# Performance work log

Hardware: AMD Instinct MI355X
Metric: run time of the kernel (lower is better)

The kernel has to match this reference:

```python
import itertools
import jax, jax.numpy as jnp
import numpy as np

B, RES, H, KD, DIM = 16, (32, 32), 16, 128, 2048
N = RES[0] * RES[1]          # 1024 tokens
D = KD                       # per-head dim (attn_ratio=1)
DH = H * D                   # 2048
QKV_OUT = 3 * DH             # 6144
SCALE = KD ** -0.5
LN_EPS = 1e-5


def _make_bias_idxs():
    points = list(itertools.product(range(RES[0]), range(RES[1])))
    offsets = {}
    idxs = []
    for p1 in points:
        for p2 in points:
            off = (abs(p1[0] - p2[0]), abs(p1[1] - p2[1]))
            if off not in offsets:
                offsets[off] = len(offsets)
            idxs.append(offsets[off])
    return np.array(idxs, dtype=np.int32).reshape(N, N), len(offsets)


def setup_inputs() -> dict:
    key = jax.random.key(0)
    ks = jax.random.split(key, 6)
    idxs_np, n_off = _make_bias_idxs()  # n_off == 1024 for 32x32
    return {
        "x": jax.random.normal(ks[0], (B, N, DIM), jnp.float32),
        "ln_gamma": jnp.ones((DIM,), jnp.float32),
        "ln_beta": jnp.zeros((DIM,), jnp.float32),
        "qkv_w": jax.random.normal(ks[1], (DIM, QKV_OUT), jnp.float32) * (DIM ** -0.5),
        "qkv_b": jnp.zeros((QKV_OUT,), jnp.float32),
        "proj_w": jax.random.normal(ks[2], (DH, DIM), jnp.float32) * (DH ** -0.5),
        "proj_b": jnp.zeros((DIM,), jnp.float32),
        "attention_biases": jax.random.normal(ks[3], (H, n_off), jnp.float32) * 0.02,
        "bias_idxs": jnp.asarray(idxs_np),
    }


def reference(x, ln_gamma, ln_beta, qkv_w, qkv_b, proj_w, proj_b,
              attention_biases, bias_idxs):
    # LayerNorm over last dim
    mu = jnp.mean(x, axis=-1, keepdims=True)
    var = jnp.mean(jnp.square(x - mu), axis=-1, keepdims=True)
    xn = (x - mu) * jax.lax.rsqrt(var + LN_EPS) * ln_gamma + ln_beta

    qkv = xn @ qkv_w + qkv_b                      # [B, N, 3*H*D]
    qkv = qkv.reshape(B, N, 3, H, D).transpose(2, 0, 3, 1, 4)  # [3, B, H, N, D]
    q, k, v = qkv[0], qkv[1], qkv[2]

    attn = jnp.einsum('bhid,bhjd->bhij', q, k) * SCALE  # [B, H, N, N]
    bias = attention_biases[:, bias_idxs]               # gather -> [H, N, N]
    attn = jax.nn.softmax(attn + bias, axis=-1)

    out = jnp.einsum('bhij,bhjd->bhid', attn, v)        # [B, H, N, D]
    out = out.transpose(0, 2, 1, 3).reshape(B, N, DH)   # b n (h d)
    return out @ proj_w + proj_b
```

## Files before the change

### kernel.cpp

```cpp
#include <hip/hip_runtime.h>


typedef __attribute__((ext_vector_type(4)))  float          f32x4;
typedef __attribute__((ext_vector_type(16))) float          f32x16;
typedef __attribute__((ext_vector_type(8)))  short          bf16x8;
typedef __attribute__((ext_vector_type(8)))  unsigned short u16x8;
typedef __attribute__((ext_vector_type(4)))  unsigned short u16x4;

#define DEV __device__ __forceinline__

DEV unsigned short f2bf(float f) {
  union { float f; unsigned int u; } v; v.f = f;
  unsigned int r = v.u + 0x7fffu + ((v.u >> 16) & 1u);
  return (unsigned short)(r >> 16);
}

DEV f32x4 mfma16(bf16x8 a, bf16x8 b, f32x4 c) {
  return __builtin_amdgcn_mfma_f32_16x16x32_bf16(a, b, c, 0, 0, 0);
}
DEV f32x16 mfma32(bf16x8 a, bf16x8 b, f32x16 c) {
  return __builtin_amdgcn_mfma_f32_32x32x16_bf16(a, b, c, 0, 0, 0);
}

#define GLD_LDS16(g, l) __builtin_amdgcn_global_load_lds(                      \
    (const __attribute__((address_space(1))) void*)(g),                        \
    (__attribute__((address_space(3))) void*)(l), 16, 0, 0)

__global__ __launch_bounds__(256) void ln_kernel(
    const float* __restrict__ x, const float* __restrict__ gam,
    const float* __restrict__ bet, unsigned short* __restrict__ xn)
{
  const int row = blockIdx.x;
  const int t   = threadIdx.x;
  const f32x4* xr = (const f32x4*)(x + (size_t)row * 2048);
  f32x4 v0 = xr[t * 2], v1 = xr[t * 2 + 1];
  float s = 0.f, ss = 0.f;
#pragma unroll
  for (int i = 0; i < 4; ++i) { s += v0[i]; ss += v0[i] * v0[i]; }
#pragma unroll
  for (int i = 0; i < 4; ++i) { s += v1[i]; ss += v1[i] * v1[i]; }
#pragma unroll
  for (int off = 32; off; off >>= 1) {
    s  += __shfl_xor(s, off);
    ss += __shfl_xor(ss, off);
  }
  __shared__ float r0[4], r1[4];
  const int w = t >> 6, lane = t & 63;
  if (lane == 0) { r0[w] = s; r1[w] = ss; }
  __syncthreads();
  s  = r0[0] + r0[1] + r0[2] + r0[3];
  ss = r1[0] + r1[1] + r1[2] + r1[3];
  const float mu = s * (1.f / 2048.f);
  const float rs = rsqrtf(ss * (1.f / 2048.f) - mu * mu + 1e-5f);
  const f32x4* gr = (const f32x4*)gam;
  const f32x4* br = (const f32x4*)bet;
  f32x4 g0 = gr[t * 2], g1 = gr[t * 2 + 1];
  f32x4 b0 = br[t * 2], b1 = br[t * 2 + 1];
  u16x8 o;
#pragma unroll
  for (int i = 0; i < 4; ++i) o[i]     = f2bf((v0[i] - mu) * rs * g0[i] + b0[i]);
#pragma unroll
  for (int i = 0; i < 4; ++i) o[4 + i] = f2bf((v1[i] - mu) * rs * g1[i] + b1[i]);
  *(u16x8*)(xn + (size_t)row * 2048 + t * 8) = o;
}

__global__ __launch_bounds__(256) void wtrans(
    const float* __restrict__ W, unsigned short* __restrict__ Wt, int K, int C)
{
  __shared__ float tile[32][33];
  const int c0 = blockIdx.x * 32, k0 = blockIdx.y * 32;
  const int t = threadIdx.x;
  const int r8 = t >> 5, c32 = t & 31;
#pragma unroll
  for (int i = 0; i < 4; ++i)
    tile[i * 8 + r8][c32] = W[(size_t)(k0 + i * 8 + r8) * C + c0 + c32];
  __syncthreads();
#pragma unroll
  for (int i = 0; i < 4; ++i)
    Wt[(size_t)(c0 + i * 8 + r8) * K + k0 + c32] = f2bf(tile[c32][i * 8 + r8]);
}

template <int EPI>
__global__ __launch_bounds__(256, 2) void gemm_nt(
    const unsigned short* __restrict__ A, const unsigned short* __restrict__ Wt,
    const float* __restrict__ bias, void* __restrict__ o0,
    void* __restrict__ o1, void* __restrict__ o2, int K, int C)
{
  __shared__ unsigned short lds[2][2][8192];
  const int nwg   = gridDim.x * gridDim.y;
  const int chunk = nwg >> 3;
  int flat = blockIdx.y * gridDim.x + blockIdx.x;
  flat = (flat & 7) * chunk + (flat >> 3);
  const int m0 = (flat / gridDim.x) * 128;
  const int n0 = (flat % gridDim.x) * 128;
  const int tid = threadIdx.x, lane = tid & 63, w = tid >> 6;
  const int lhi = lane >> 4, llo = lane & 15;
  const int wr = w >> 1, wc = w & 1;

  const unsigned short* Ab = A  + (size_t)m0 * K;
  const unsigned short* Bb = Wt + (size_t)n0 * K;

  f32x4 acc[4][4];
#pragma unroll
  for (int i = 0; i < 4; ++i)
#pragma unroll
    for (int j = 0; j < 4; ++j) { acc[i][j][0] = 0; acc[i][j][1] = 0; acc[i][j][2] = 0; acc[i][j][3] = 0; }

  auto stage = [&](int kt, int buf) {
    const int k0 = kt * 64;
#pragma unroll
    for (int i = 0; i < 4; ++i) {
      const int c    = w * 4 + i;
      const int row  = c * 8 + (lane >> 3);
      const int colb = (lane & 7) * 16;
      const int scol = (colb ^ ((row & 7) << 4)) >> 1;
      GLD_LDS16(Ab + (size_t)row * K + k0 + scol, &lds[buf][0][c * 512]);
      GLD_LDS16(Bb + (size_t)row * K + k0 + scol, &lds[buf][1][c * 512]);
    }
  };

  stage(0, 0);
  __syncthreads();
  const int nk = K >> 6;
  int cur = 0;
  for (int kt = 0; kt < nk; ++kt) {
    if (kt + 1 < nk) stage(kt + 1, cur ^ 1);
    const char* aL = (const char*)&lds[cur][0][0];
    const char* bL = (const char*)&lds[cur][1][0];
#pragma unroll
    for (int kk = 0; kk < 2; ++kk) {
      const int kb = kk * 64 + lhi * 16;
      bf16x8 af[4], bf[4];
#pragma unroll
      for (int t2 = 0; t2 < 4; ++t2) {
        const int ra = wr * 64 + t2 * 16 + llo;
        af[t2] = *(const bf16x8*)(aL + ra * 128 + (kb ^ ((ra & 7) << 4)));
        const int rb = wc * 64 + t2 * 16 + llo;
        bf[t2] = *(const bf16x8*)(bL + rb * 128 + (kb ^ ((rb & 7) << 4)));
      }
#pragma unroll
      for (int ai = 0; ai < 4; ++ai)
#pragma unroll
        for (int bj = 0; bj < 4; ++bj)
          acc[ai][bj] = mfma16(af[ai], bf[bj], acc[ai][bj]);
    }
    __syncthreads();
    cur ^= 1;
  }

  if (EPI == 0) {
    unsigned short* q  = (unsigned short*)o0;
    unsigned short* kk = (unsigned short*)o1;
    unsigned short* vT = (unsigned short*)o2;
    const int which = n0 >> 11;
    const int h     = (n0 >> 7) & 15;
#pragma unroll
    for (int bj = 0; bj < 4; ++bj) {
      const int c  = n0 + wc * 64 + bj * 16 + llo;
      const float bv = bias[c];
      const int d  = c & 127;
#pragma unroll
      for (int ai = 0; ai < 4; ++ai) {
        const int m = m0 + wr * 64 + ai * 16 + lhi * 4;
        const int b = m >> 10, n = m & 1023;
        if (which == 2) {
          u16x4 pk;
#pragma unroll
          for (int r = 0; r < 4; ++r) pk[r] = f2bf(acc[ai][bj][r] + bv);
          *(u16x4*)(vT + ((size_t)(b * 16 + h) * 128 + d) * 1024 + n) = pk;
        } else {
          unsigned short* dst = (which == 0) ? q : kk;
          const float sc = (which == 0) ? 0.08838834764831845f : 1.0f;
#pragma unroll
          for (int r = 0; r < 4; ++r)
            dst[((size_t)(b * 16 + h) * 1024 + n + r) * 128 + d] =
                f2bf((acc[ai][bj][r] + bv) * sc);
        }
      }
    }
  } else {
    float* fo = (float*)o0;
#pragma unroll
    for (int bj = 0; bj < 4; ++bj) {
      const int c  = n0 + wc * 64 + bj * 16 + llo;
      const float bv = bias[c];
#pragma unroll
      for (int ai = 0; ai < 4; ++ai) {
        const int m = m0 + wr * 64 + ai * 16 + lhi * 4;
#pragma unroll
        for (int r = 0; r < 4; ++r)
          fo[(size_t)(m + r) * C + c] = acc[ai][bj][r] + bv;
      }
    }
  }
}

__global__ __launch_bounds__(256) void attn4(
    const unsigned short* __restrict__ q, const unsigned short* __restrict__ k,
    const unsigned short* __restrict__ vT, const float* __restrict__ biases,
    unsigned short* __restrict__ aout, int n_off)
{
  __shared__ unsigned short kt[2][8192];
  __shared__ unsigned short vt[2][8192];
  __shared__ float brow_s[1024];

  const int bid0 = blockIdx.x;
  const int id = ((bid0 & 7) << 8) + (bid0 >> 3);
  const int qt = id & 7, bh = id >> 3;
  const int h = bh & 15, b = bh >> 4;
  const int tid = threadIdx.x, lane = tid & 63, w = tid >> 6;
  const int c = lane & 31, hi = lane >> 5;

  const size_t hd = (size_t)bh * (1024 * 128);
  const unsigned short* qp = q  + hd;
  const unsigned short* kp = k  + hd;
  const unsigned short* vp = vT + hd;
  const int qbase = qt * 128 + w * 32;
  const int qrow  = qbase + c;
  const int qru   = qbase >> 5;
  const int qc    = c;

  for (int i = tid; i < n_off; i += 256) brow_s[i] = biases[(size_t)h * n_off + i];

  bf16x8 qf[8];
#pragma unroll
  for (int kd = 0; kd < 8; ++kd)
    qf[kd] = *(const bf16x8*)(qp + (size_t)qrow * 128 + kd * 16 + hi * 8);

  int adc[16];
#pragma unroll
  for (int r = 0; r < 16; ++r) {
    const int cj = (r & 3) + 8 * (r >> 2) + 4 * hi;
    const int d  = qc - cj;
    adc[r] = d < 0 ? -d : d;
  }

  f32x16 o_[4];
#pragma unroll
  for (int ds = 0; ds < 4; ++ds)
#pragma unroll
    for (int r = 0; r < 16; ++r) o_[ds][r] = 0.f;
  float m_ = -1e30f, l_ = 0.f;

  auto stageK = [&](int jt_, int buf) {
    const int j0g = jt_ << 6;
#pragma unroll
    for (int i = 0; i < 4; ++i) {
      const int cc = w * 4 + i;
      const int r2 = cc * 8 + (lane >> 3);
      const int cb = (lane & 7) * 16;
      const int j  = r2 >> 1, dh = r2 & 1;
      const int sc = (cb ^ ((j & 7) << 4)) >> 1;
      GLD_LDS16(kp + (size_t)(j0g + j) * 128 + dh * 64 + sc, &kt[buf][cc * 512]);
    }
  };
  auto stageV = [&](int jt_, int buf) {
    const int j0g = jt_ << 6;
#pragma unroll
    for (int i = 0; i < 4; ++i) {
      const int cc = w * 4 + i;
      const int d  = cc * 8 + (lane >> 3);
      const int cb = (lane & 7) * 16;
      const int sc = (cb ^ ((d & 7) << 4)) >> 1;
      GLD_LDS16(vp + (size_t)d * 1024 + j0g + sc, &vt[buf][cc * 512]);
    }
  };

  stageK(0, 0);
  stageV(0, 0);
  __syncthreads();

  int cur = 0;
  for (int jt = 0; jt < 16; ++jt) {
    if (jt < 15) { stageK(jt + 1, cur ^ 1); stageV(jt + 1, cur ^ 1); }

    const char* kb_ = (const char*)&kt[cur][0];
    f32x16 s0, s1;
#pragma unroll
    for (int r = 0; r < 16; ++r) { s0[r] = 0.f; s1[r] = 0.f; }
    __builtin_amdgcn_s_setprio(1);
#pragma unroll
    for (int kd = 0; kd < 8; ++kd) {
      const int dlo = kd * 16 + hi * 8;
      const int off = (((dlo & 63) * 2) ^ ((c & 7) << 4));
      bf16x8 kf0 = *(const bf16x8*)(kb_ + (((c)      << 1) | (dlo >> 6)) * 128 + off);
      bf16x8 kf1 = *(const bf16x8*)(kb_ + (((32 + c) << 1) | (dlo >> 6)) * 128 + off);
      s0 = mfma32(kf0, qf[kd], s0);
      s1 = mfma32(kf1, qf[kd], s1);
    }
    __builtin_amdgcn_s_setprio(0);

    float sv[2][16];
#pragma unroll
    for (int js = 0; js < 2; ++js) {
      const int drr = qru - (jt * 2 + js);
      const int adr = (drr < 0 ? -drr : drr) * 32;
#pragma unroll
      for (int r = 0; r < 16; ++r)
        sv[js][r] = (js ? s1[r] : s0[r]) + brow_s[adr + adc[r]];
    }

    float mx = sv[0][0];
#pragma unroll
    for (int r = 1; r < 16; ++r) mx = fmaxf(mx, sv[0][r]);
#pragma unroll
    for (int r = 0; r < 16; ++r) mx = fmaxf(mx, sv[1][r]);
    mx = fmaxf(mx, __shfl_xor(mx, 32));

    if (!__all(mx - m_ <= 8.0f)) {
      const float nm  = fmaxf(m_, mx);
      const float fac = __expf(m_ - nm);
      m_ = nm;
      l_ *= fac;
#pragma unroll
      for (int r = 0; r < 16; ++r) {
        const float fr = __shfl(fac, (r & 3) + 8 * (r >> 2) + 4 * hi);
#pragma unroll
        for (int ds = 0; ds < 4; ++ds) o_[ds][r] *= fr;
      }
    }

    float sum = 0.f;
#pragma unroll
    for (int js = 0; js < 2; ++js)
#pragma unroll
      for (int r = 0; r < 16; ++r) {
        const float p = __expf(sv[js][r] - m_);
        sv[js][r] = p;
        sum += p;
      }
    sum += __shfl_xor(sum, 32);
    l_ += sum;

    unsigned int wpk[2][8];
#pragma unroll
    for (int js = 0; js < 2; ++js)
#pragma unroll
      for (int wi = 0; wi < 8; ++wi)
        wpk[js][wi] = (unsigned int)f2bf(sv[js][2 * wi]) |
                      ((unsigned int)f2bf(sv[js][2 * wi + 1]) << 16);

    const char* vb_ = (const char*)&vt[cur][0];
    __builtin_amdgcn_s_setprio(1);
#pragma unroll
    for (int kj = 0; kj < 4; ++kj) {
      const int js = kj >> 1, base = (kj & 1) * 4;
      const unsigned int u0 = wpk[js][base + 0], u1 = wpk[js][base + 1];
      const unsigned int u2 = wpk[js][base + 2], u3 = wpk[js][base + 3];
      const unsigned int t0 = __shfl_xor(u0, 32), t1 = __shfl_xor(u1, 32);
      const unsigned int t2 = __shfl_xor(u2, 32), t3 = __shfl_xor(u3, 32);
      union { unsigned int u[4]; bf16x8 v; } af;
      af.u[0] = hi ? t2 : u0;
      af.u[1] = hi ? t3 : u1;
      af.u[2] = hi ? u2 : t0;
      af.u[3] = hi ? u3 : t1;
#pragma unroll
      for (int ds = 0; ds < 4; ++ds) {
        const int d = ds * 32 + c;
        bf16x8 vf = *(const bf16x8*)(vb_ + d * 128 + ((kj * 32 + hi * 16) ^ ((d & 7) << 4)));
        o_[ds] = mfma32(af.v, vf, o_[ds]);
      }
    }
    __builtin_amdgcn_s_setprio(0);

    __syncthreads();
    cur ^= 1;
  }

#pragma unroll
  for (int r = 0; r < 16; ++r) {
    const int qloc = (r & 3) + 8 * (r >> 2) + 4 * hi;
    const float lr = __shfl(l_, qloc);
    const float inv = 1.f / lr;
    const size_t rowb = (size_t)b * 1024 * 2048 + (size_t)(qbase + qloc) * 2048 + h * 128;
#pragma unroll
    for (int ds = 0; ds < 4; ++ds)
      aout[rowb + ds * 32 + c] = f2bf(o_[ds][r] * inv);
  }
}

extern "C" void kernel_launch(void* const* d_in, const int* in_sizes, int n_in,
                              void* d_out, int out_size, void* d_ws, size_t ws_size,
                              hipStream_t stream)
{
  const float* x      = (const float*)d_in[0];
  const float* ln_g   = (const float*)d_in[1];
  const float* ln_b   = (const float*)d_in[2];
  const float* qkv_w  = (const float*)d_in[3];
  const float* qkv_b  = (const float*)d_in[4];
  const float* proj_w = (const float*)d_in[5];
  const float* proj_b = (const float*)d_in[6];
  const float* ab     = (const float*)d_in[7];
  float* out = (float*)d_out;
  char* ws = (char*)d_ws;

  unsigned short* xn = (unsigned short*)(ws);
  unsigned short* wt = (unsigned short*)(ws + (size_t)64  * 1024 * 1024);
  unsigned short* qb = (unsigned short*)(ws + (size_t)88  * 1024 * 1024);
  unsigned short* kb = (unsigned short*)(ws + (size_t)152 * 1024 * 1024);
  unsigned short* vb = (unsigned short*)(ws + (size_t)216 * 1024 * 1024);
  const int n_off = in_sizes[7] / 16;

  ln_kernel<<<16384, 256, 0, stream>>>(x, ln_g, ln_b, xn);
  wtrans<<<dim3(6144 / 32, 2048 / 32), 256, 0, stream>>>(qkv_w, wt, 2048, 6144);
  gemm_nt<0><<<dim3(48, 128), 256, 0, stream>>>(xn, wt, qkv_b, qb, kb, vb, 2048, 6144);
  wtrans<<<dim3(2048 / 32, 2048 / 32), 256, 0, stream>>>(proj_w, wt, 2048, 2048);
  attn4<<<2048, 256, 0, stream>>>(qb, kb, vb, ab, xn, n_off);
  gemm_nt<1><<<dim3(16, 128), 256, 0, stream>>>(xn, wt, proj_b, out, nullptr, nullptr, 2048, 2048);
}
```

Measured before the change: 1.326 ms.

## Enlarge GEMM tiles to 256x256 with 8 waves and ping-pong staged pipeline

Both bf16 GEMMs move from 128x128 tiles with 4 waves to 256x256 tiles with 8 waves. The main loop is split into four sub-phases, and each sub-phase interleaves LDS fragment reads, staging of the next A halves and the B tile two steps ahead, and MFMA bursts. Explicit barriers, vmcnt and lgkmcnt waits and s_setprio bracket each phase. The aim is more data reuse per loaded byte and better overlap of global-to-LDS loads with matrix math. In exchange it uses 128KB of LDS and more accumulator registers, which may limit occupancy, and it leaves fewer blocks per launch.

```diff
diff --git a/kernel.cpp b/kernel.cpp
--- a/kernel.cpp
+++ b/kernel.cpp
@@ -81,71 +81,161 @@
 }
 
 template <int EPI>
-__global__ __launch_bounds__(256, 2) void gemm_nt(
+__global__ __launch_bounds__(512, 2) void gemm_nt(
     const unsigned short* __restrict__ A, const unsigned short* __restrict__ Wt,
     const float* __restrict__ bias, void* __restrict__ o0,
     void* __restrict__ o1, void* __restrict__ o2, int K, int C)
 {
-  __shared__ unsigned short lds[2][2][8192];
+  __shared__ unsigned short Al[2][256 * 64];
+  __shared__ unsigned short Bl[2][256 * 64];
+
   const int nwg   = gridDim.x * gridDim.y;
   const int chunk = nwg >> 3;
   int flat = blockIdx.y * gridDim.x + blockIdx.x;
   flat = (flat & 7) * chunk + (flat >> 3);
-  const int m0 = (flat / gridDim.x) * 128;
-  const int n0 = (flat % gridDim.x) * 128;
+  const int m0 = (flat / gridDim.x) * 256;
+  const int n0 = (flat % gridDim.x) * 256;
   const int tid = threadIdx.x, lane = tid & 63, w = tid >> 6;
   const int lhi = lane >> 4, llo = lane & 15;
-  const int wr = w >> 1, wc = w & 1;
+  const int wr = w >> 2, wc = w & 3;
 
   const unsigned short* Ab = A  + (size_t)m0 * K;
   const unsigned short* Bb = Wt + (size_t)n0 * K;
 
-  f32x4 acc[4][4];
-#pragma unroll
-  for (int i = 0; i < 4; ++i)
+  f32x4 acc[8][4];
+#pragma unroll
+  for (int i = 0; i < 8; ++i)
 #pragma unroll
     for (int j = 0; j < 4; ++j) { acc[i][j][0] = 0; acc[i][j][1] = 0; acc[i][j][2] = 0; acc[i][j][3] = 0; }
 
-  auto stage = [&](int kt, int buf) {
+  auto stageA = [&](int kt, int bufi, int half) {
     const int k0 = kt * 64;
 #pragma unroll
-    for (int i = 0; i < 4; ++i) {
-      const int c    = w * 4 + i;
-      const int row  = c * 8 + (lane >> 3);
-      const int colb = (lane & 7) * 16;
-      const int scol = (colb ^ ((row & 7) << 4)) >> 1;
-      GLD_LDS16(Ab + (size_t)row * K + k0 + scol, &lds[buf][0][c * 512]);
-      GLD_LDS16(Bb + (size_t)row * K + k0 + scol, &lds[buf][1][c * 512]);
+    for (int i = 0; i < 2; ++i) {
+      const int rbase = half * 128 + i * 64 + w * 8;
+      const int row   = rbase + (lane >> 3);
+      const int sc    = (((lane & 7) * 16) ^ ((row & 7) << 4)) >> 1;
+      GLD_LDS16(Ab + (size_t)row * K + k0 + sc, &Al[bufi][rbase * 64]);
     }
   };
-
-  stage(0, 0);
-  __syncthreads();
+  auto stageB = [&](int kt, int bufi, int half) {
+    const int k0 = kt * 64;
+#pragma unroll
+    for (int i = 0; i < 2; ++i) {
+      const int rbase = half * 128 + i * 64 + w * 8;
+      const int row   = rbase + (lane >> 3);
+      const int sc    = (((lane & 7) * 16) ^ ((row & 7) << 4)) >> 1;
+      GLD_LDS16(Bb + (size_t)row * K + k0 + sc, &Bl[bufi][rbase * 64]);
+    }
+  };
+
   const int nk = K >> 6;
-  int cur = 0;
-  for (int kt = 0; kt < nk; ++kt) {
-    if (kt + 1 < nk) stage(kt + 1, cur ^ 1);
-    const char* aL = (const char*)&lds[cur][0][0];
-    const char* bL = (const char*)&lds[cur][1][0];
-#pragma unroll
-    for (int kk = 0; kk < 2; ++kk) {
-      const int kb = kk * 64 + lhi * 16;
-      bf16x8 af[4], bf[4];
-#pragma unroll
-      for (int t2 = 0; t2 < 4; ++t2) {
-        const int ra = wr * 64 + t2 * 16 + llo;
-        af[t2] = *(const bf16x8*)(aL + ra * 128 + (kb ^ ((ra & 7) << 4)));
-        const int rb = wc * 64 + t2 * 16 + llo;
-        bf[t2] = *(const bf16x8*)(bL + rb * 128 + (kb ^ ((rb & 7) << 4)));
-      }
-#pragma unroll
-      for (int ai = 0; ai < 4; ++ai)
-#pragma unroll
-        for (int bj = 0; bj < 4; ++bj)
-          acc[ai][bj] = mfma16(af[ai], bf[bj], acc[ai][bj]);
-    }
-    __syncthreads();
-    cur ^= 1;
+
+  stageA(0, 0, 0); stageA(0, 0, 1);
+  stageB(0, 0, 0); stageB(0, 0, 1);
+  stageB(1, 1, 0); stageB(1, 1, 1);
+  asm volatile("s_waitcnt vmcnt(4)" ::: "memory");
+  __builtin_amdgcn_sched_barrier(0);
+  __builtin_amdgcn_s_barrier();
+
+  bf16x8 aq[4][2];
+  bf16x8 bq[4][2];
+
+  for (int t = 0; t < nk; ++t) {
+    const int buf = t & 1;
+    const char* aL = (const char*)&Al[buf][0];
+    const char* bL = (const char*)&Bl[buf][0];
+
+#pragma unroll
+    for (int rr = 0; rr < 4; ++rr)
+#pragma unroll
+      for (int kk = 0; kk < 2; ++kk) {
+        const int ra = wr * 128 + rr * 16 + llo;
+        aq[rr][kk] = *(const bf16x8*)(aL + ra * 128 + ((kk * 64 + lhi * 16) ^ ((ra & 7) << 4)));
+      }
+#pragma unroll
+    for (int nn = 0; nn < 2; ++nn)
+#pragma unroll
+      for (int kk = 0; kk < 2; ++kk) {
+        const int rb = wc * 64 + nn * 16 + llo;
+        bq[nn][kk] = *(const bf16x8*)(bL + rb * 128 + ((kk * 64 + lhi * 16) ^ ((rb & 7) << 4)));
+      }
+    if (t + 1 < nk) stageA(t + 1, (t + 1) & 1, 0);
+    __builtin_amdgcn_s_barrier();
+    asm volatile("s_waitcnt lgkmcnt(0)" ::: "memory");
+    __builtin_amdgcn_sched_barrier(0);
+    __builtin_amdgcn_s_setprio(1);
+#pragma unroll
+    for (int rr = 0; rr < 4; ++rr)
+#pragma unroll
+      for (int nn = 0; nn < 2; ++nn)
+#pragma unroll
+        for (int kk = 0; kk < 2; ++kk)
+          acc[rr][nn] = mfma16(aq[rr][kk], bq[nn][kk], acc[rr][nn]);
+    __builtin_amdgcn_s_setprio(0);
+    __builtin_amdgcn_s_barrier();
+
+#pragma unroll
+    for (int nn = 2; nn < 4; ++nn)
+#pragma unroll
+      for (int kk = 0; kk < 2; ++kk) {
+        const int rb = wc * 64 + nn * 16 + llo;
+        bq[nn][kk] = *(const bf16x8*)(bL + rb * 128 + ((kk * 64 + lhi * 16) ^ ((rb & 7) << 4)));
+      }
+    if (t + 1 < nk) stageA(t + 1, (t + 1) & 1, 1);
+    __builtin_amdgcn_s_barrier();
+    asm volatile("s_waitcnt lgkmcnt(0)" ::: "memory");
+    __builtin_amdgcn_sched_barrier(0);
+    __builtin_amdgcn_s_setprio(1);
+#pragma unroll
+    for (int rr = 0; rr < 4; ++rr)
+#pragma unroll
+      for (int nn = 2; nn < 4; ++nn)
+#pragma unroll
+        for (int kk = 0; kk < 2; ++kk)
+          acc[rr][nn] = mfma16(aq[rr][kk], bq[nn][kk], acc[rr][nn]);
+    __builtin_amdgcn_s_setprio(0);
+    __builtin_amdgcn_s_barrier();
+
+#pragma unroll
+    for (int rr = 0; rr < 4; ++rr)
+#pragma unroll
+      for (int kk = 0; kk < 2; ++kk) {
+        const int ra = wr * 128 + 64 + rr * 16 + llo;
+        aq[rr][kk] = *(const bf16x8*)(aL + ra * 128 + ((kk * 64 + lhi * 16) ^ ((ra & 7) << 4)));
+      }
+    if (t + 2 < nk) stageB(t + 2, buf, 0);
+    __builtin_amdgcn_s_barrier();
+    asm volatile("s_waitcnt lgkmcnt(0)" ::: "memory");
+    __builtin_amdgcn_sched_barrier(0);
+    __builtin_amdgcn_s_setprio(1);
+#pragma unroll
+    for (int rr = 0; rr < 4; ++rr)
+#pragma unroll
+      for (int nn = 0; nn < 2; ++nn)
+#pragma unroll
+        for (int kk = 0; kk < 2; ++kk)
+          acc[4 + rr][nn] = mfma16(aq[rr][kk], bq[nn][kk], acc[4 + rr][nn]);
+    __builtin_amdgcn_s_setprio(0);
+    __builtin_amdgcn_s_barrier();
+
+    if (t + 2 < nk) stageB(t + 2, buf, 1);
+    __builtin_amdgcn_s_barrier();
+    __builtin_amdgcn_s_setprio(1);
+#pragma unroll
+    for (int rr = 0; rr < 4; ++rr)
+#pragma unroll
+      for (int nn = 2; nn < 4; ++nn)
+#pragma unroll
+        for (int kk = 0; kk < 2; ++kk)
+          acc[4 + rr][nn] = mfma16(aq[rr][kk], bq[nn][kk], acc[4 + rr][nn]);
+    __builtin_amdgcn_s_setprio(0);
+    if (t + 1 < nk) {
+      if (t + 2 < nk) asm volatile("s_waitcnt vmcnt(4)" ::: "memory");
+      else            asm volatile("s_waitcnt vmcnt(0)" ::: "memory");
+      __builtin_amdgcn_sched_barrier(0);
+    }
+    __builtin_amdgcn_s_barrier();
   }
 
   if (EPI == 0) {
@@ -153,43 +243,43 @@
     unsigned short* kk = (unsigned short*)o1;
     unsigned short* vT = (unsigned short*)o2;
     const int which = n0 >> 11;
-    const int h     = (n0 >> 7) & 15;
-#pragma unroll
-    for (int bj = 0; bj < 4; ++bj) {
-      const int c  = n0 + wc * 64 + bj * 16 + llo;
+#pragma unroll
+    for (int n = 0; n < 4; ++n) {
+      const int c  = n0 + wc * 64 + n * 16 + llo;
       const float bv = bias[c];
+      const int h  = (c >> 7) & 15;
       const int d  = c & 127;
 #pragma unroll
-      for (int ai = 0; ai < 4; ++ai) {
-        const int m = m0 + wr * 64 + ai * 16 + lhi * 4;
-        const int b = m >> 10, n = m & 1023;
+      for (int r = 0; r < 8; ++r) {
+        const int m = m0 + wr * 128 + r * 16 + lhi * 4;
+        const int b = m >> 10, ntok = m & 1023;
         if (which == 2) {
           u16x4 pk;
 #pragma unroll
-          for (int r = 0; r < 4; ++r) pk[r] = f2bf(acc[ai][bj][r] + bv);
-          *(u16x4*)(vT + ((size_t)(b * 16 + h) * 128 + d) * 1024 + n) = pk;
+          for (int e = 0; e < 4; ++e) pk[e] = f2bf(acc[r][n][e] + bv);
+          *(u16x4*)(vT + ((size_t)(b * 16 + h) * 128 + d) * 1024 + ntok) = pk;
         } else {
           unsigned short* dst = (which == 0) ? q : kk;
           const float sc = (which == 0) ? 0.08838834764831845f : 1.0f;
 #pragma unroll
-          for (int r = 0; r < 4; ++r)
-            dst[((size_t)(b * 16 + h) * 1024 + n + r) * 128 + d] =
-                f2bf((acc[ai][bj][r] + bv) * sc);
+          for (int e = 0; e < 4; ++e)
+            dst[((size_t)(b * 16 + h) * 1024 + ntok + e) * 128 + d] =
+                f2bf((acc[r][n][e] + bv) * sc);
         }
       }
     }
   } else {
     float* fo = (float*)o0;
 #pragma unroll
-    for (int bj = 0; bj < 4; ++bj) {
-      const int c  = n0 + wc * 64 + bj * 16 + llo;
+    for (int n = 0; n < 4; ++n) {
+      const int c  = n0 + wc * 64 + n * 16 + llo;
       const float bv = bias[c];
 #pragma unroll
-      for (int ai = 0; ai < 4; ++ai) {
-        const int m = m0 + wr * 64 + ai * 16 + lhi * 4;
-#pragma unroll
-        for (int r = 0; r < 4; ++r)
-          fo[(size_t)(m + r) * C + c] = acc[ai][bj][r] + bv;
+      for (int r = 0; r < 8; ++r) {
+        const int m = m0 + wr * 128 + r * 16 + lhi * 4;
+#pragma unroll
+        for (int e = 0; e < 4; ++e)
+          fo[(size_t)(m + e) * C + c] = acc[r][n][e] + bv;
       }
     }
   }
@@ -403,8 +493,8 @@
 
   ln_kernel<<<16384, 256, 0, stream>>>(x, ln_g, ln_b, xn);
   wtrans<<<dim3(6144 / 32, 2048 / 32), 256, 0, stream>>>(qkv_w, wt, 2048, 6144);
-  gemm_nt<0><<<dim3(48, 128), 256, 0, stream>>>(xn, wt, qkv_b, qb, kb, vb, 2048, 6144);
+  gemm_nt<0><<<dim3(24, 64), 512, 0, stream>>>(xn, wt, qkv_b, qb, kb, vb, 2048, 6144);
   wtrans<<<dim3(2048 / 32, 2048 / 32), 256, 0, stream>>>(proj_w, wt, 2048, 2048);
   attn4<<<2048, 256, 0, stream>>>(qb, kb, vb, ab, xn, n_off);
-  gemm_nt<1><<<dim3(16, 128), 256, 0, stream>>>(xn, wt, proj_b, out, nullptr, nullptr, 2048, 2048);
-}
+  gemm_nt<1><<<dim3(8, 64), 512, 0, stream>>>(xn, wt, proj_b, out, nullptr, nullptr, 2048, 2048);
+}
```

Measured after the change: 1.218 ms. -8.2%, faster.
